# Optimization experiments

Hardware: AMD Instinct MI355X
Metric: run time of the kernel (lower is better)

Reference implementation:

```python
import jax, jax.numpy as jnp
import numpy as np

DROPOUT_P = 0.5  # used as an additive constant in the normalizers, not as dropout
N = 384


def setup_inputs() -> dict:
    key = jax.random.key(0)
    k1, k2 = jax.random.split(key)
    inp = jax.random.uniform(k1, (N, N, N), dtype=jnp.float32)
    w = jax.random.uniform(k2, (N, N, N), dtype=jnp.float32)
    return {"input": inp, "w": w}


def reference(input, w):
    # e[i,j,l] = sum_k input[i,j,k] * w[l,k,j]
    e = jnp.einsum('ijk,lkj->ijl', input, w)
    # k (normalized by input row-sums) is dead code in the original forward;
    # only q and v feed the output, so we skip it.
    v = e  # second identical einsum in the source
    s_in = input.sum(axis=-1, keepdims=True)          # [N, N, 1]
    # einsum('ijk,ijl->ijl', input, w) == (sum_k input) * w
    q = s_in * w
    q = q / (DROPOUT_P + w.sum(axis=-1, keepdims=True))
    # causal mask: strict upper triangle set to -inf, broadcast over batch
    mask = jnp.triu(jnp.full((N, N), -jnp.inf, dtype=q.dtype), k=1)  # [N, N]
    attn = jax.nn.softmax(q + mask[None, :, :], axis=-1)              # [N, N, N]
    return jnp.matmul(attn, v)
```

## Files before the change

### kernel.cpp

```cpp
#include <hip/hip_runtime.h>
#include <hip/hip_bf16.h>


#define N 384
#define N2 (N * N)
#define BK 64
static const size_t N3 = (size_t)N * N * N;

typedef __attribute__((ext_vector_type(8))) short s16x8;
typedef __attribute__((ext_vector_type(4))) float f32x4;

#define AS1 __attribute__((address_space(1)))
#define AS3 __attribute__((address_space(3)))
__device__ __forceinline__ void gll16(const void* g, void* l) {
    __builtin_amdgcn_global_load_lds((const AS1 unsigned int*)g,
                                     (AS3 unsigned int*)l, 16, 0, 0);
}
#define WAITL0 asm volatile("s_waitcnt lgkmcnt(0)" ::: "memory")
#define BAR    __builtin_amdgcn_s_barrier()

__device__ __forceinline__ unsigned short f32_to_bf16(float f) {
    unsigned int u = __float_as_uint(f);
    u += 0x7FFFu + ((u >> 16) & 1u);
    return (unsigned short)(u >> 16);
}
__device__ __forceinline__ unsigned int pk2(float a, float b) {
    return (unsigned int)f32_to_bf16(a) | ((unsigned int)f32_to_bf16(b) << 16);
}

__global__ __launch_bounds__(256) void kT(const float* __restrict__ w,
                                          unsigned short* __restrict__ wt) {
    __shared__ unsigned short tile[64][68];
    const int r0 = blockIdx.x * 64;
    const int j0 = blockIdx.y * 64;
    const int tx = threadIdx.x & 63;
    const int ty = threadIdx.x >> 6;
#pragma unroll
    for (int p = 0; p < 16; ++p) {
        const int r = ty * 16 + p;
        tile[r][tx] = f32_to_bf16(w[(size_t)(r0 + r) * N + j0 + tx]);
    }
    __syncthreads();
#pragma unroll
    for (int p = 0; p < 16; ++p) {
        const int jj = ty * 16 + p;
        wt[(size_t)(j0 + jj) * N2 + r0 + tx] = tile[tx][jj];
    }
}

__global__ __launch_bounds__(256, 4) void k_e3(const float* __restrict__ in,
                                               const unsigned short* __restrict__ wt,
                                               unsigned short* __restrict__ e,
                                               float* __restrict__ rs) {
    __shared__ union {
        struct { unsigned short A[64 * 64]; unsigned short B[2][128 * 64]; } s;
        unsigned short C[64 * 136];
    } sm;

    const int lin = blockIdx.x;
    const int swz = (lin & 7) * 864 + (lin >> 3);
    const int j   = swz / 18;
    const int sub = swz % 18;
    const int i0  = (sub / 3) * 64;
    const int l0  = (sub % 3) * 128;

    const int t = threadIdx.x, lane = t & 63, wv = t >> 6;
    const int fr = lane & 15, fx = lane >> 4;
    const int wr = (wv >> 1) * 32;
    const int wc = (wv & 1) * 64;
    const int rb_off = lane >> 3;
    const int p8     = lane & 7;

    const int ra = t >> 2, ca = (t & 3) * 2;
    const float* Ab = in + (size_t)(i0 + ra) * N2 + (size_t)j * N + ca * 8;
    unsigned short* AsW0 = sm.s.A + ra * 64 + (((ca + 0) ^ (ra & 7)) * 8);
    unsigned short* AsW1 = sm.s.A + ra * 64 + (((ca + 1) ^ (ra & 7)) * 8);

    const unsigned short* Wj = wt + (size_t)j * N2 + (size_t)l0 * N;

    f32x4 acc[2][4];
#pragma unroll
    for (int m = 0; m < 2; ++m)
#pragma unroll
        for (int n = 0; n < 4; ++n) acc[m][n] = (f32x4){0.f, 0.f, 0.f, 0.f};

    float rsum = 0.f;

    float4 va[4];
    va[0] = *(const float4*)(Ab);
    va[1] = *(const float4*)(Ab + 4);
    va[2] = *(const float4*)(Ab + 8);
    va[3] = *(const float4*)(Ab + 12);

    {
        unsigned short* B0 = sm.s.B[0];
#pragma unroll
        for (int op = 0; op < 4; ++op) {
            const int rr = wv * 32 + op * 8 + rb_off;
            const int sc = p8 ^ (rr & 7);
            gll16(Wj + (size_t)rr * N + sc * 8, B0 + (wv * 32 + op * 8) * 64);
        }
        asm volatile("s_waitcnt vmcnt(0)" ::: "memory");
    }

    unsigned short* Bc = sm.s.B[0];
    unsigned short* Bn = sm.s.B[1];

#pragma unroll
    for (int tt = 0; tt < 6; ++tt) {
        rsum += (va[0].x + va[0].y + va[0].z + va[0].w) +
                (va[1].x + va[1].y + va[1].z + va[1].w) +
                (va[2].x + va[2].y + va[2].z + va[2].w) +
                (va[3].x + va[3].y + va[3].z + va[3].w);
        {
            uint4 a0, a1;
            a0.x = pk2(va[0].x, va[0].y); a0.y = pk2(va[0].z, va[0].w);
            a0.z = pk2(va[1].x, va[1].y); a0.w = pk2(va[1].z, va[1].w);
            a1.x = pk2(va[2].x, va[2].y); a1.y = pk2(va[2].z, va[2].w);
            a1.z = pk2(va[3].x, va[3].y); a1.w = pk2(va[3].z, va[3].w);
            *(uint4*)AsW0 = a0;
            *(uint4*)AsW1 = a1;
        }
        if (tt < 5) {
            const int kn = (tt + 1) * 64;
#pragma unroll
            for (int op = 0; op < 4; ++op) {
                const int rr = wv * 32 + op * 8 + rb_off;
                const int sc = p8 ^ (rr & 7);
                gll16(Wj + (size_t)rr * N + kn + sc * 8, Bn + (wv * 32 + op * 8) * 64);
            }
            __builtin_amdgcn_sched_barrier(0);
            const float* An = Ab + kn;
            va[0] = *(const float4*)(An);
            va[1] = *(const float4*)(An + 4);
            va[2] = *(const float4*)(An + 8);
            va[3] = *(const float4*)(An + 12);
        }
        WAITL0;
        BAR;
        __builtin_amdgcn_s_setprio(1);
#pragma unroll
        for (int kk = 0; kk < 2; ++kk) {
            s16x8 af[2], bf[4];
#pragma unroll
            for (int m = 0; m < 2; ++m) {
                const int row = wr + m * 16 + fr;
                const int x   = (kk * 4 + fx) ^ (row & 7);
                af[m] = *(const s16x8*)(sm.s.A + row * 64 + x * 8);
            }
#pragma unroll
            for (int n = 0; n < 4; ++n) {
                const int row = wc + n * 16 + fr;
                const int x   = (kk * 4 + fx) ^ (row & 7);
                bf[n] = *(const s16x8*)(Bc + row * 64 + x * 8);
            }
#pragma unroll
            for (int m = 0; m < 2; ++m)
#pragma unroll
                for (int n = 0; n < 4; ++n)
                    acc[m][n] = __builtin_amdgcn_mfma_f32_16x16x32_bf16(
                        af[m], bf[n], acc[m][n], 0, 0, 0);
        }
        __builtin_amdgcn_s_setprio(0);
        if (tt < 5) {
            asm volatile("s_waitcnt vmcnt(4)" ::: "memory");
        }
        BAR;
        unsigned short* tp = Bc; Bc = Bn; Bn = tp;
    }

    rsum += __shfl_xor(rsum, 1, 64);
    rsum += __shfl_xor(rsum, 2, 64);
    if (rs != nullptr && l0 == 0 && (t & 3) == 0)
        rs[(size_t)(i0 + ra) * N + j] = rsum;

    __syncthreads();
    const int rq = fx * 4;
#pragma unroll
    for (int m = 0; m < 2; ++m)
#pragma unroll
        for (int n = 0; n < 4; ++n)
#pragma unroll
            for (int r = 0; r < 4; ++r)
                sm.C[(wr + m * 16 + rq + r) * 136 + wc + n * 16 + fr] =
                    f32_to_bf16(acc[m][n][r]);
    __syncthreads();
#pragma unroll
    for (int it = 0; it < 4; ++it) {
        const int cid = it * 256 + t;
        const int row = cid >> 4;
        const int c   = cid & 15;
        *(uint4*)(e + (size_t)(i0 + row) * N2 + (size_t)j * N + l0 + c * 8) =
            *(const uint4*)&sm.C[row * 136 + c * 8];
    }
}

__global__ __launch_bounds__(256) void k_eT(const unsigned short* __restrict__ e,
                                            unsigned short* __restrict__ et) {
    __shared__ unsigned short tile[64][68];
    const int m0 = blockIdx.x * 64, l0 = blockIdx.y * 64;
    const size_t ib = (size_t)blockIdx.z * N2;
    const int t  = threadIdx.x;
    const int c4 = (t & 15) * 4, r = t >> 4;
#pragma unroll
    for (int p = 0; p < 4; ++p) {
        ushort4 v = *(const ushort4*)(e + ib + (size_t)(m0 + r + 16 * p) * N + l0 + c4);
        tile[c4 + 0][r + 16 * p] = v.x;
        tile[c4 + 1][r + 16 * p] = v.y;
        tile[c4 + 2][r + 16 * p] = v.z;
        tile[c4 + 3][r + 16 * p] = v.w;
    }
    __syncthreads();
#pragma unroll
    for (int p = 0; p < 4; ++p) {
        const int lr = r + 16 * p;
        ushort4 v = *(const ushort4*)&tile[lr][c4];
        *(ushort4*)(et + ib + (size_t)(l0 + lr) * N + m0 + c4) = v;
    }
}

template <bool HAVE_RS>
__global__ __launch_bounds__(256) void k_attn(const float* __restrict__ in,
                                              const float* __restrict__ w,
                                              const float* __restrict__ rs,
                                              unsigned short* __restrict__ attn) {
    const int row  = blockIdx.x * 4 + (threadIdx.x >> 6);
    const int lane = threadIdx.x & 63;
    const int jr   = row % N;

    const float2* wp = (const float2*)(w + (size_t)row * N);

    float2 wv[3];
    float rs_in = 0.f, rs_w = 0.f;
#pragma unroll
    for (int c = 0; c < 3; ++c) {
        wv[c] = wp[lane + 64 * c];
        rs_w += wv[c].x + wv[c].y;
    }
    if (HAVE_RS) {
#pragma unroll
        for (int s = 1; s < 64; s <<= 1) rs_w += __shfl_xor(rs_w, s, 64);
        rs_in = rs[row];
    } else {
        const float2* ip = (const float2*)(in + (size_t)row * N);
#pragma unroll
        for (int c = 0; c < 3; ++c) {
            float2 iv = ip[lane + 64 * c];
            rs_in += iv.x + iv.y;
        }
#pragma unroll
        for (int s = 1; s < 64; s <<= 1) {
            rs_in += __shfl_xor(rs_in, s, 64);
            rs_w  += __shfl_xor(rs_w, s, 64);
        }
    }
    const float scale = rs_in / (0.5f + rs_w);

    float2 q[3];
    float mx = -INFINITY;
#pragma unroll
    for (int c = 0; c < 3; ++c) {
        const int l = (lane + 64 * c) * 2;
        q[c].x = (l     <= jr) ? scale * wv[c].x : -INFINITY;
        q[c].y = (l + 1 <= jr) ? scale * wv[c].y : -INFINITY;
        mx = fmaxf(mx, fmaxf(q[c].x, q[c].y));
    }
#pragma unroll
    for (int s = 1; s < 64; s <<= 1) mx = fmaxf(mx, __shfl_xor(mx, s, 64));

    float2 p[3];
    float sum = 0.f;
#pragma unroll
    for (int c = 0; c < 3; ++c) {
        const int l = (lane + 64 * c) * 2;
        p[c].x = (l     <= jr) ? exp2f((q[c].x - mx) * 1.44269504f) : 0.f;
        p[c].y = (l + 1 <= jr) ? exp2f((q[c].y - mx) * 1.44269504f) : 0.f;
        sum += p[c].x + p[c].y;
    }
#pragma unroll
    for (int s = 1; s < 64; s <<= 1) sum += __shfl_xor(sum, s, 64);
    const float inv = 1.f / sum;
    unsigned int* ap = (unsigned int*)(attn + (size_t)row * N);
#pragma unroll
    for (int c = 0; c < 3; ++c)
        ap[lane + 64 * c] = pk2(p[c].x * inv, p[c].y * inv);
}

__global__ __launch_bounds__(256, 4) void k_av3(const unsigned short* __restrict__ attn,
                                                const unsigned short* __restrict__ et,
                                                float* __restrict__ out) {
    __shared__ union {
        struct { unsigned short A[64 * 64]; unsigned short B[2][128 * 64]; } s;
        float C[64 * 132];
    } sm;

    const int lin = blockIdx.x;
    const int swz = (lin & 7) * 864 + (lin >> 3);
    const int i   = swz / 18;
    const int sub = swz % 18;
    const int j0  = (sub / 3) * 64;
    const int l0  = (sub % 3) * 128;
    const int nt  = (j0 >> 6) + 1;

    const int t = threadIdx.x, lane = t & 63, wv = t >> 6;
    const int fr = lane & 15, fx = lane >> 4;
    const int wr = (wv >> 1) * 32;
    const int wc = (wv & 1) * 64;
    const int rb_off = lane >> 3;
    const int p8     = lane & 7;

    const int ra = t >> 2, ca = (t & 3) * 2;
    const unsigned short* Ab = attn + (size_t)i * N2 + (size_t)(j0 + ra) * N + ca * 8;
    unsigned short* AsW0 = sm.s.A + ra * 64 + (((ca + 0) ^ (ra & 7)) * 8);
    unsigned short* AsW1 = sm.s.A + ra * 64 + (((ca + 1) ^ (ra & 7)) * 8);

    const unsigned short* Bg = et + (size_t)i * N2 + (size_t)l0 * N;

    f32x4 acc[2][4];
#pragma unroll
    for (int m = 0; m < 2; ++m)
#pragma unroll
        for (int n = 0; n < 4; ++n) acc[m][n] = (f32x4){0.f, 0.f, 0.f, 0.f};

    uint4 va0 = *(const uint4*)(Ab);
    uint4 va1 = *(const uint4*)(Ab + 8);

    {
        unsigned short* B0 = sm.s.B[0];
#pragma unroll
        for (int op = 0; op < 4; ++op) {
            const int rr = wv * 32 + op * 8 + rb_off;
            const int sc = p8 ^ (rr & 7);
            gll16(Bg + (size_t)rr * N + sc * 8, B0 + (wv * 32 + op * 8) * 64);
        }
        asm volatile("s_waitcnt vmcnt(0)" ::: "memory");
    }

    unsigned short* Bc = sm.s.B[0];
    unsigned short* Bn = sm.s.B[1];

    for (int tt = 0; tt < nt; ++tt) {
        *(uint4*)AsW0 = va0;
        *(uint4*)AsW1 = va1;
        if (tt + 1 < nt) {
            const int kn = (tt + 1) * 64;
#pragma unroll
            for (int op = 0; op < 4; ++op) {
                const int rr = wv * 32 + op * 8 + rb_off;
                const int sc = p8 ^ (rr & 7);
                gll16(Bg + (size_t)rr * N + kn + sc * 8, Bn + (wv * 32 + op * 8) * 64);
            }
            __builtin_amdgcn_sched_barrier(0);
            va0 = *(const uint4*)(Ab + kn);
            va1 = *(const uint4*)(Ab + kn + 8);
        }
        WAITL0;
        BAR;
        __builtin_amdgcn_s_setprio(1);
#pragma unroll
        for (int kk = 0; kk < 2; ++kk) {
            s16x8 af[2], bf[4];
#pragma unroll
            for (int m = 0; m < 2; ++m) {
                const int row = wr + m * 16 + fr;
                const int x   = (kk * 4 + fx) ^ (row & 7);
                af[m] = *(const s16x8*)(sm.s.A + row * 64 + x * 8);
            }
#pragma unroll
            for (int n = 0; n < 4; ++n) {
                const int row = wc + n * 16 + fr;
                const int x   = (kk * 4 + fx) ^ (row & 7);
                bf[n] = *(const s16x8*)(Bc + row * 64 + x * 8);
            }
#pragma unroll
            for (int m = 0; m < 2; ++m)
#pragma unroll
                for (int n = 0; n < 4; ++n)
                    acc[m][n] = __builtin_amdgcn_mfma_f32_16x16x32_bf16(
                        af[m], bf[n], acc[m][n], 0, 0, 0);
        }
        __builtin_amdgcn_s_setprio(0);
        if (tt + 1 < nt) {
            asm volatile("s_waitcnt vmcnt(2)" ::: "memory");
        }
        BAR;
        unsigned short* tp = Bc; Bc = Bn; Bn = tp;
    }

    __syncthreads();
    const int rq = fx * 4;
#pragma unroll
    for (int m = 0; m < 2; ++m)
#pragma unroll
        for (int n = 0; n < 4; ++n)
#pragma unroll
            for (int r = 0; r < 4; ++r)
                sm.C[(wr + m * 16 + rq + r) * 132 + wc + n * 16 + fr] = acc[m][n][r];
    __syncthreads();
#pragma unroll
    for (int it = 0; it < 8; ++it) {
        const int cid = it * 256 + t;
        const int row = cid >> 5;
        const int c   = cid & 31;
        *(float4*)(out + (size_t)i * N2 + (size_t)(j0 + row) * N + l0 + c * 4) =
            *(const float4*)&sm.C[row * 132 + c * 4];
    }
}

extern "C" void kernel_launch(void* const* d_in, const int* in_sizes, int n_in,
                              void* d_out, int out_size, void* d_ws, size_t ws_size,
                              hipStream_t stream) {
    const float* in = (const float*)d_in[0];
    const float* w  = (const float*)d_in[1];
    float* out      = (float*)d_out;

    unsigned short* r0 = (unsigned short*)d_ws;
    unsigned short* r1 = (unsigned short*)d_ws + N3;
    const bool have_rs = ws_size >= 2 * N3 * sizeof(unsigned short) + (size_t)N2 * sizeof(float);
    float* rs = have_rs ? (float*)((unsigned short*)d_ws + 2 * N3) : nullptr;

    kT<<<dim3(N2 / 64, N / 64), 256, 0, stream>>>(w, r0);
    k_e3<<<dim3(6912), 256, 0, stream>>>(in, r0, r1, rs);
    k_eT<<<dim3(6, 6, N), 256, 0, stream>>>(r1, r0);
    if (have_rs)
        k_attn<true><<<dim3(N2 / 4), 256, 0, stream>>>(in, w, rs, r1);
    else
        k_attn<false><<<dim3(N2 / 4), 256, 0, stream>>>(in, w, nullptr, r1);
    k_av3<<<dim3(6912), 256, 0, stream>>>(r1, r0, out);
}
```

Baseline: 392.9 us.

## Single-buffer B tiles and shrink epilogue staging to fit more blocks per CU

Both GEMM kernels drop the double-buffered B tile in LDS and load the current k-slice directly before computing, with a barrier at the loop top to protect reuse. The AV kernel also writes its fp32 output tile in two half-height phases so the C staging buffer is halved. Launch bounds are raised to 5 blocks per CU. The aim is higher occupancy to hide latency across blocks, at the cost of losing intra-block overlap of B loads with MFMA work.

```diff
diff --git a/kernel.cpp b/kernel.cpp
--- a/kernel.cpp
+++ b/kernel.cpp
@@ -16,8 +16,7 @@
     __builtin_amdgcn_global_load_lds((const AS1 unsigned int*)g,
                                      (AS3 unsigned int*)l, 16, 0, 0);
 }
-#define WAITL0 asm volatile("s_waitcnt lgkmcnt(0)" ::: "memory")
-#define BAR    __builtin_amdgcn_s_barrier()
+#define BAR __builtin_amdgcn_s_barrier()
 
 __device__ __forceinline__ unsigned short f32_to_bf16(float f) {
     unsigned int u = __float_as_uint(f);
@@ -48,12 +47,12 @@
     }
 }
 
-__global__ __launch_bounds__(256, 4) void k_e3(const float* __restrict__ in,
+__global__ __launch_bounds__(256, 5) void k_e4(const float* __restrict__ in,
                                                const unsigned short* __restrict__ wt,
                                                unsigned short* __restrict__ e,
                                                float* __restrict__ rs) {
     __shared__ union {
-        struct { unsigned short A[64 * 64]; unsigned short B[2][128 * 64]; } s;
+        struct { unsigned short A[64 * 64]; unsigned short B[128 * 64]; } s;
         unsigned short C[64 * 136];
     } sm;
 
@@ -92,22 +91,10 @@
     va[2] = *(const float4*)(Ab + 8);
     va[3] = *(const float4*)(Ab + 12);
 
-    {
-        unsigned short* B0 = sm.s.B[0];
-#pragma unroll
-        for (int op = 0; op < 4; ++op) {
-            const int rr = wv * 32 + op * 8 + rb_off;
-            const int sc = p8 ^ (rr & 7);
-            gll16(Wj + (size_t)rr * N + sc * 8, B0 + (wv * 32 + op * 8) * 64);
-        }
-        asm volatile("s_waitcnt vmcnt(0)" ::: "memory");
-    }
-
-    unsigned short* Bc = sm.s.B[0];
-    unsigned short* Bn = sm.s.B[1];
-
 #pragma unroll
     for (int tt = 0; tt < 6; ++tt) {
+        const int k0 = tt * 64;
+        BAR;
         rsum += (va[0].x + va[0].y + va[0].z + va[0].w) +
                 (va[1].x + va[1].y + va[1].z + va[1].w) +
                 (va[2].x + va[2].y + va[2].z + va[2].w) +
@@ -121,22 +108,24 @@
             *(uint4*)AsW0 = a0;
             *(uint4*)AsW1 = a1;
         }
+#pragma unroll
+        for (int op = 0; op < 4; ++op) {
+            const int rr = wv * 32 + op * 8 + rb_off;
+            const int sc = p8 ^ (rr & 7);
+            gll16(Wj + (size_t)rr * N + k0 + sc * 8,
+                  sm.s.B + (wv * 32 + op * 8) * 64);
+        }
+        __builtin_amdgcn_sched_barrier(0);
         if (tt < 5) {
-            const int kn = (tt + 1) * 64;
-#pragma unroll
-            for (int op = 0; op < 4; ++op) {
-                const int rr = wv * 32 + op * 8 + rb_off;
-                const int sc = p8 ^ (rr & 7);
-                gll16(Wj + (size_t)rr * N + kn + sc * 8, Bn + (wv * 32 + op * 8) * 64);
-            }
-            __builtin_amdgcn_sched_barrier(0);
-            const float* An = Ab + kn;
+            const float* An = Ab + k0 + 64;
             va[0] = *(const float4*)(An);
             va[1] = *(const float4*)(An + 4);
             va[2] = *(const float4*)(An + 8);
             va[3] = *(const float4*)(An + 12);
-        }
-        WAITL0;
+            asm volatile("s_waitcnt vmcnt(4) lgkmcnt(0)" ::: "memory");
+        } else {
+            asm volatile("s_waitcnt vmcnt(0) lgkmcnt(0)" ::: "memory");
+        }
         BAR;
         __builtin_amdgcn_s_setprio(1);
 #pragma unroll
@@ -152,7 +141,7 @@
             for (int n = 0; n < 4; ++n) {
                 const int row = wc + n * 16 + fr;
                 const int x   = (kk * 4 + fx) ^ (row & 7);
-                bf[n] = *(const s16x8*)(Bc + row * 64 + x * 8);
+                bf[n] = *(const s16x8*)(sm.s.B + row * 64 + x * 8);
             }
 #pragma unroll
             for (int m = 0; m < 2; ++m)
@@ -162,11 +151,6 @@
                         af[m], bf[n], acc[m][n], 0, 0, 0);
         }
         __builtin_amdgcn_s_setprio(0);
-        if (tt < 5) {
-            asm volatile("s_waitcnt vmcnt(4)" ::: "memory");
-        }
-        BAR;
-        unsigned short* tp = Bc; Bc = Bn; Bn = tp;
     }
 
     rsum += __shfl_xor(rsum, 1, 64);
@@ -286,12 +270,12 @@
         ap[lane + 64 * c] = pk2(p[c].x * inv, p[c].y * inv);
 }
 
-__global__ __launch_bounds__(256, 4) void k_av3(const unsigned short* __restrict__ attn,
+__global__ __launch_bounds__(256, 5) void k_av4(const unsigned short* __restrict__ attn,
                                                 const unsigned short* __restrict__ et,
                                                 float* __restrict__ out) {
     __shared__ union {
-        struct { unsigned short A[64 * 64]; unsigned short B[2][128 * 64]; } s;
-        float C[64 * 132];
+        struct { unsigned short A[64 * 64]; unsigned short B[128 * 64]; } s;
+        float C[32 * 132];
     } sm;
 
     const int lin = blockIdx.x;
@@ -325,36 +309,27 @@
     uint4 va0 = *(const uint4*)(Ab);
     uint4 va1 = *(const uint4*)(Ab + 8);
 
-    {
-        unsigned short* B0 = sm.s.B[0];
+    for (int tt = 0; tt < nt; ++tt) {
+        const int k0 = tt * 64;
+        BAR;
+        *(uint4*)AsW0 = va0;
+        *(uint4*)AsW1 = va1;
 #pragma unroll
         for (int op = 0; op < 4; ++op) {
             const int rr = wv * 32 + op * 8 + rb_off;
             const int sc = p8 ^ (rr & 7);
-            gll16(Bg + (size_t)rr * N + sc * 8, B0 + (wv * 32 + op * 8) * 64);
-        }
-        asm volatile("s_waitcnt vmcnt(0)" ::: "memory");
-    }
-
-    unsigned short* Bc = sm.s.B[0];
-    unsigned short* Bn = sm.s.B[1];
-
-    for (int tt = 0; tt < nt; ++tt) {
-        *(uint4*)AsW0 = va0;
-        *(uint4*)AsW1 = va1;
+            gll16(Bg + (size_t)rr * N + k0 + sc * 8,
+                  sm.s.B + (wv * 32 + op * 8) * 64);
+        }
+        __builtin_amdgcn_sched_barrier(0);
         if (tt + 1 < nt) {
-            const int kn = (tt + 1) * 64;
-#pragma unroll
-            for (int op = 0; op < 4; ++op) {
-                const int rr = wv * 32 + op * 8 + rb_off;
-                const int sc = p8 ^ (rr & 7);
-                gll16(Bg + (size_t)rr * N + kn + sc * 8, Bn + (wv * 32 + op * 8) * 64);
-            }
-            __builtin_amdgcn_sched_barrier(0);
+            const int kn = k0 + 64;
             va0 = *(const uint4*)(Ab + kn);
             va1 = *(const uint4*)(Ab + kn + 8);
-        }
-        WAITL0;
+            asm volatile("s_waitcnt vmcnt(2) lgkmcnt(0)" ::: "memory");
+        } else {
+            asm volatile("s_waitcnt vmcnt(0) lgkmcnt(0)" ::: "memory");
+        }
         BAR;
         __builtin_amdgcn_s_setprio(1);
 #pragma unroll
@@ -370,7 +345,7 @@
             for (int n = 0; n < 4; ++n) {
                 const int row = wc + n * 16 + fr;
                 const int x   = (kk * 4 + fx) ^ (row & 7);
-                bf[n] = *(const s16x8*)(Bc + row * 64 + x * 8);
+                bf[n] = *(const s16x8*)(sm.s.B + row * 64 + x * 8);
             }
 #pragma unroll
             for (int m = 0; m < 2; ++m)
@@ -380,30 +355,31 @@
                         af[m], bf[n], acc[m][n], 0, 0, 0);
         }
         __builtin_amdgcn_s_setprio(0);
-        if (tt + 1 < nt) {
-            asm volatile("s_waitcnt vmcnt(2)" ::: "memory");
-        }
-        BAR;
-        unsigned short* tp = Bc; Bc = Bn; Bn = tp;
-    }
-
-    __syncthreads();
+    }
+
     const int rq = fx * 4;
 #pragma unroll
-    for (int m = 0; m < 2; ++m)
-#pragma unroll
-        for (int n = 0; n < 4; ++n)
-#pragma unroll
-            for (int r = 0; r < 4; ++r)
-                sm.C[(wr + m * 16 + rq + r) * 132 + wc + n * 16 + fr] = acc[m][n][r];
-    __syncthreads();
-#pragma unroll
-    for (int it = 0; it < 8; ++it) {
-        const int cid = it * 256 + t;
-        const int row = cid >> 5;
-        const int c   = cid & 31;
-        *(float4*)(out + (size_t)i * N2 + (size_t)(j0 + row) * N + l0 + c * 4) =
-            *(const float4*)&sm.C[row * 132 + c * 4];
+    for (int ph = 0; ph < 2; ++ph) {
+        __syncthreads();
+        if ((wv >> 1) == ph) {
+#pragma unroll
+            for (int m = 0; m < 2; ++m)
+#pragma unroll
+                for (int n = 0; n < 4; ++n)
+#pragma unroll
+                    for (int r = 0; r < 4; ++r)
+                        sm.C[(m * 16 + rq + r) * 132 + wc + n * 16 + fr] =
+                            acc[m][n][r];
+        }
+        __syncthreads();
+#pragma unroll
+        for (int it = 0; it < 4; ++it) {
+            const int cid = it * 256 + t;
+            const int row = cid >> 5;
+            const int c   = cid & 31;
+            *(float4*)(out + (size_t)i * N2 + (size_t)(j0 + ph * 32 + row) * N + l0 + c * 4) =
+                *(const float4*)&sm.C[row * 132 + c * 4];
+        }
     }
 }
 
@@ -420,11 +396,11 @@
     float* rs = have_rs ? (float*)((unsigned short*)d_ws + 2 * N3) : nullptr;
 
     kT<<<dim3(N2 / 64, N / 64), 256, 0, stream>>>(w, r0);
-    k_e3<<<dim3(6912), 256, 0, stream>>>(in, r0, r1, rs);
+    k_e4<<<dim3(6912), 256, 0, stream>>>(in, r0, r1, rs);
     k_eT<<<dim3(6, 6, N), 256, 0, stream>>>(r1, r0);
     if (have_rs)
         k_attn<true><<<dim3(N2 / 4), 256, 0, stream>>>(in, w, rs, r1);
     else
         k_attn<false><<<dim3(N2 / 4), 256, 0, stream>>>(in, w, nullptr, r1);
-    k_av3<<<dim3(6912), 256, 0, stream>>>(r1, r0, out);
-}
+    k_av4<<<dim3(6912), 256, 0, stream>>>(r1, r0, out);
+}
```

Result: slower. 453.3 us (+15.4%).

## Enlarge batched-GEMM tile to 128x192 and drop B double buffering

Applied to the files above, without the earlier changes.

The e-computation kernel now computes a 128x192 output tile per block (4x6 MFMA fragments per wave) instead of 64x128, cutting the grid from 6912 to 2304 blocks. The aim is more operand reuse per LDS load and less redundant global traffic. To fit LDS and registers, B is single-buffered with plain __syncthreads, prefetch overlap and setprio are removed, and the epilogue writes in two halves through a smaller C buffer. The trade-off is lower occupancy (launch bounds 3) and less overlap of loads with MFMA work.

```diff
diff --git a/kernel.cpp b/kernel.cpp
--- a/kernel.cpp
+++ b/kernel.cpp
@@ -48,41 +48,40 @@
     }
 }
 
-__global__ __launch_bounds__(256, 4) void k_e3(const float* __restrict__ in,
+__global__ __launch_bounds__(256, 3) void k_e5(const float* __restrict__ in,
                                                const unsigned short* __restrict__ wt,
                                                unsigned short* __restrict__ e,
                                                float* __restrict__ rs) {
     __shared__ union {
-        struct { unsigned short A[64 * 64]; unsigned short B[2][128 * 64]; } s;
-        unsigned short C[64 * 136];
+        struct { unsigned short A[128 * 64]; unsigned short B[192 * 64]; } s;
+        unsigned short C[64 * 200];
     } sm;
 
     const int lin = blockIdx.x;
-    const int swz = (lin & 7) * 864 + (lin >> 3);
-    const int j   = swz / 18;
-    const int sub = swz % 18;
-    const int i0  = (sub / 3) * 64;
-    const int l0  = (sub % 3) * 128;
+    const int swz = (lin & 7) * 288 + (lin >> 3);
+    const int j   = swz / 6;
+    const int sub = swz % 6;
+    const int i0  = (sub >> 1) * 128;
+    const int l0  = (sub & 1) * 192;
 
     const int t = threadIdx.x, lane = t & 63, wv = t >> 6;
     const int fr = lane & 15, fx = lane >> 4;
-    const int wr = (wv >> 1) * 32;
-    const int wc = (wv & 1) * 64;
+    const int wr = (wv >> 1) * 64;
+    const int wc = (wv & 1) * 96;
     const int rb_off = lane >> 3;
     const int p8     = lane & 7;
 
-    const int ra = t >> 2, ca = (t & 3) * 2;
-    const float* Ab = in + (size_t)(i0 + ra) * N2 + (size_t)j * N + ca * 8;
-    unsigned short* AsW0 = sm.s.A + ra * 64 + (((ca + 0) ^ (ra & 7)) * 8);
-    unsigned short* AsW1 = sm.s.A + ra * 64 + (((ca + 1) ^ (ra & 7)) * 8);
+    const int ra = t >> 1, cb = (t & 1) * 4;
+    const float* Ab = in + (size_t)(i0 + ra) * N2 + (size_t)j * N + cb * 8;
+    unsigned short* AsRow = sm.s.A + ra * 64;
 
     const unsigned short* Wj = wt + (size_t)j * N2 + (size_t)l0 * N;
 
-    f32x4 acc[2][4];
-#pragma unroll
-    for (int m = 0; m < 2; ++m)
-#pragma unroll
-        for (int n = 0; n < 4; ++n) acc[m][n] = (f32x4){0.f, 0.f, 0.f, 0.f};
+    f32x4 acc[4][6];
+#pragma unroll
+    for (int m = 0; m < 4; ++m)
+#pragma unroll
+        for (int n = 0; n < 6; ++n) acc[m][n] = (f32x4){0.f, 0.f, 0.f, 0.f};
 
     float rsum = 0.f;
 
@@ -92,106 +91,107 @@
     va[2] = *(const float4*)(Ab + 8);
     va[3] = *(const float4*)(Ab + 12);
 
-    {
-        unsigned short* B0 = sm.s.B[0];
-#pragma unroll
-        for (int op = 0; op < 4; ++op) {
-            const int rr = wv * 32 + op * 8 + rb_off;
-            const int sc = p8 ^ (rr & 7);
-            gll16(Wj + (size_t)rr * N + sc * 8, B0 + (wv * 32 + op * 8) * 64);
-        }
-        asm volatile("s_waitcnt vmcnt(0)" ::: "memory");
-    }
-
-    unsigned short* Bc = sm.s.B[0];
-    unsigned short* Bn = sm.s.B[1];
-
 #pragma unroll
     for (int tt = 0; tt < 6; ++tt) {
-        rsum += (va[0].x + va[0].y + va[0].z + va[0].w) +
-                (va[1].x + va[1].y + va[1].z + va[1].w) +
-                (va[2].x + va[2].y + va[2].z + va[2].w) +
-                (va[3].x + va[3].y + va[3].z + va[3].w);
+        const int k0 = tt * 64;
+        __syncthreads();
         {
+            rsum += (va[0].x + va[0].y + va[0].z + va[0].w) +
+                    (va[1].x + va[1].y + va[1].z + va[1].w) +
+                    (va[2].x + va[2].y + va[2].z + va[2].w) +
+                    (va[3].x + va[3].y + va[3].z + va[3].w);
             uint4 a0, a1;
             a0.x = pk2(va[0].x, va[0].y); a0.y = pk2(va[0].z, va[0].w);
             a0.z = pk2(va[1].x, va[1].y); a0.w = pk2(va[1].z, va[1].w);
             a1.x = pk2(va[2].x, va[2].y); a1.y = pk2(va[2].z, va[2].w);
             a1.z = pk2(va[3].x, va[3].y); a1.w = pk2(va[3].z, va[3].w);
-            *(uint4*)AsW0 = a0;
-            *(uint4*)AsW1 = a1;
+            *(uint4*)(AsRow + (((cb + 0) ^ (ra & 7)) * 8)) = a0;
+            *(uint4*)(AsRow + (((cb + 1) ^ (ra & 7)) * 8)) = a1;
+        }
+        {
+            float4 w0 = *(const float4*)(Ab + k0 + 16);
+            float4 w1 = *(const float4*)(Ab + k0 + 20);
+            float4 w2 = *(const float4*)(Ab + k0 + 24);
+            float4 w3 = *(const float4*)(Ab + k0 + 28);
+            rsum += (w0.x + w0.y + w0.z + w0.w) +
+                    (w1.x + w1.y + w1.z + w1.w) +
+                    (w2.x + w2.y + w2.z + w2.w) +
+                    (w3.x + w3.y + w3.z + w3.w);
+            uint4 a2, a3;
+            a2.x = pk2(w0.x, w0.y); a2.y = pk2(w0.z, w0.w);
+            a2.z = pk2(w1.x, w1.y); a2.w = pk2(w1.z, w1.w);
+            a3.x = pk2(w2.x, w2.y); a3.y = pk2(w2.z, w2.w);
+            a3.z = pk2(w3.x, w3.y); a3.w = pk2(w3.z, w3.w);
+            *(uint4*)(AsRow + (((cb + 2) ^ (ra & 7)) * 8)) = a2;
+            *(uint4*)(AsRow + (((cb + 3) ^ (ra & 7)) * 8)) = a3;
+        }
+#pragma unroll
+        for (int itb = 0; itb < 6; ++itb) {
+            const int rb = wv * 48 + itb * 8 + rb_off;
+            const int sc = p8 ^ (rb & 7);
+            gll16(Wj + (size_t)rb * N + k0 + sc * 8,
+                  sm.s.B + (wv * 48 + itb * 8) * 64);
         }
         if (tt < 5) {
-            const int kn = (tt + 1) * 64;
-#pragma unroll
-            for (int op = 0; op < 4; ++op) {
-                const int rr = wv * 32 + op * 8 + rb_off;
-                const int sc = p8 ^ (rr & 7);
-                gll16(Wj + (size_t)rr * N + kn + sc * 8, Bn + (wv * 32 + op * 8) * 64);
-            }
-            __builtin_amdgcn_sched_barrier(0);
-            const float* An = Ab + kn;
+            const float* An = Ab + k0 + 64;
             va[0] = *(const float4*)(An);
             va[1] = *(const float4*)(An + 4);
             va[2] = *(const float4*)(An + 8);
             va[3] = *(const float4*)(An + 12);
         }
-        WAITL0;
-        BAR;
-        __builtin_amdgcn_s_setprio(1);
+        __syncthreads();
 #pragma unroll
         for (int kk = 0; kk < 2; ++kk) {
-            s16x8 af[2], bf[4];
-#pragma unroll
-            for (int m = 0; m < 2; ++m) {
+            s16x8 af[4], bf[6];
+#pragma unroll
+            for (int m = 0; m < 4; ++m) {
                 const int row = wr + m * 16 + fr;
                 const int x   = (kk * 4 + fx) ^ (row & 7);
                 af[m] = *(const s16x8*)(sm.s.A + row * 64 + x * 8);
             }
 #pragma unroll
-            for (int n = 0; n < 4; ++n) {
+            for (int n = 0; n < 6; ++n) {
                 const int row = wc + n * 16 + fr;
                 const int x   = (kk * 4 + fx) ^ (row & 7);
-                bf[n] = *(const s16x8*)(Bc + row * 64 + x * 8);
+                bf[n] = *(const s16x8*)(sm.s.B + row * 64 + x * 8);
             }
 #pragma unroll
-            for (int m = 0; m < 2; ++m)
-#pragma unroll
-                for (int n = 0; n < 4; ++n)
+            for (int m = 0; m < 4; ++m)
+#pragma unroll
+                for (int n = 0; n < 6; ++n)
                     acc[m][n] = __builtin_amdgcn_mfma_f32_16x16x32_bf16(
                         af[m], bf[n], acc[m][n], 0, 0, 0);
         }
-        __builtin_amdgcn_s_setprio(0);
-        if (tt < 5) {
-            asm volatile("s_waitcnt vmcnt(4)" ::: "memory");
-        }
-        BAR;
-        unsigned short* tp = Bc; Bc = Bn; Bn = tp;
     }
 
     rsum += __shfl_xor(rsum, 1, 64);
-    rsum += __shfl_xor(rsum, 2, 64);
-    if (rs != nullptr && l0 == 0 && (t & 3) == 0)
+    if (rs != nullptr && l0 == 0 && (t & 1) == 0)
         rs[(size_t)(i0 + ra) * N + j] = rsum;
 
+    const int rq = fx * 4;
     __syncthreads();
-    const int rq = fx * 4;
-#pragma unroll
-    for (int m = 0; m < 2; ++m)
-#pragma unroll
-        for (int n = 0; n < 4; ++n)
-#pragma unroll
-            for (int r = 0; r < 4; ++r)
-                sm.C[(wr + m * 16 + rq + r) * 136 + wc + n * 16 + fr] =
-                    f32_to_bf16(acc[m][n][r]);
-    __syncthreads();
-#pragma unroll
-    for (int it = 0; it < 4; ++it) {
-        const int cid = it * 256 + t;
-        const int row = cid >> 4;
-        const int c   = cid & 15;
-        *(uint4*)(e + (size_t)(i0 + row) * N2 + (size_t)j * N + l0 + c * 8) =
-            *(const uint4*)&sm.C[row * 136 + c * 8];
+#pragma unroll
+    for (int p = 0; p < 2; ++p) {
+        if ((wv >> 1) == p) {
+#pragma unroll
+            for (int m = 0; m < 4; ++m)
+#pragma unroll
+                for (int n = 0; n < 6; ++n)
+#pragma unroll
+                    for (int r = 0; r < 4; ++r)
+                        sm.C[(m * 16 + rq + r) * 200 + wc + n * 16 + fr] =
+                            f32_to_bf16(acc[m][n][r]);
+        }
+        __syncthreads();
+#pragma unroll
+        for (int it = 0; it < 6; ++it) {
+            const int cid = it * 256 + t;
+            const int row = cid / 24;
+            const int c   = cid % 24;
+            *(uint4*)(e + (size_t)(i0 + p * 64 + row) * N2 + (size_t)j * N + l0 + c * 8) =
+                *(const uint4*)&sm.C[row * 200 + c * 8];
+        }
+        if (p == 0) __syncthreads();
     }
 }
 
@@ -420,7 +420,7 @@
     float* rs = have_rs ? (float*)((unsigned short*)d_ws + 2 * N3) : nullptr;
 
     kT<<<dim3(N2 / 64, N / 64), 256, 0, stream>>>(w, r0);
-    k_e3<<<dim3(6912), 256, 0, stream>>>(in, r0, r1, rs);
+    k_e5<<<dim3(2304), 256, 0, stream>>>(in, r0, r1, rs);
     k_eT<<<dim3(6, 6, N), 256, 0, stream>>>(r1, r0);
     if (have_rs)
         k_attn<true><<<dim3(N2 / 4), 256, 0, stream>>>(in, w, rs, r1);
```

Result: slower. 528.6 us (+34.5%).
